# Optimization experiments

Hardware: AMD Instinct MI355X
Metric: run time of the kernel (lower is better)

The kernel has to match this reference:

```python
import jax, jax.numpy as jnp
import numpy as np

INPUT_SIZE = 416
NUM_CLASSES = 80
A = 3  # anchors per yolo layer
SS = [13, 26, 52]  # grid sizes (strides 32/16/8)
ANCHORS = [[(116, 90), (156, 198), (373, 326)],
           [(30, 61), (62, 45), (59, 119)],
           [(10, 13), (16, 30), (33, 23)]]
B, L = 16, 50


def _build_priors():
    boxes, cols, rows, pws, phs, szs = [], [], [], [], [], []
    for l, S in enumerate(SS):
        for i in range(S):
            for j in range(S):
                cx, cy = (j + 0.5) / S, (i + 0.5) / S
                for (aw, ah) in ANCHORS[l]:
                    w, h = aw / INPUT_SIZE, ah / INPUT_SIZE
                    boxes.append((cx - 0.5 * w, cy - 0.5 * h, w, h))
                    cols.append(j); rows.append(i)
                    pws.append(aw); phs.append(ah); szs.append(S)
    f = lambda a: np.asarray(a, np.float32)
    return f(boxes), f(cols), f(rows), f(pws), f(phs), f(szs)

PRIORS_NP, PCOL_NP, PROW_NP, PPW_NP, PPH_NP, PS_NP = _build_priors()
N = PRIORS_NP.shape[0]  # 10647
OFF = np.concatenate([[0], np.cumsum([S * S * A for S in SS])])


def setup_inputs() -> dict:
    key = jax.random.key(0)
    ks = jax.random.split(key, 8)
    inp = {}
    for l, S in enumerate(SS):
        inp[f"yolo_out{l}"] = jax.random.normal(ks[l], (B, A * (NUM_CLASSES + 5), S, S), jnp.float32)
    cls = jax.random.randint(ks[3], (B, L), 0, NUM_CLASSES).astype(jnp.float32)
    valid = jax.random.uniform(ks[4], (B, L)) < 0.4
    cls = jnp.where(valid, cls, -1.0)  # class < 0 means padding label
    xy = jax.random.uniform(ks[5], (B, L, 2), minval=0.0, maxval=0.7)
    wh = jax.random.uniform(ks[6], (B, L, 2), minval=0.05, maxval=0.3)
    inp["labels"] = jnp.concatenate([cls[..., None], xy, wh], axis=-1)[:, None]  # [B,1,L,5]
    return inp


def _bce(p, t):
    # torch BCELoss (mean) with the same log clamp at -100
    lg = lambda x: jnp.maximum(jnp.log(x), -100.0)
    return jnp.mean(-(t * lg(p) + (1.0 - t) * lg(1.0 - p)))


def _build_targets(labels):
    pri = jnp.asarray(PRIORS_NP)
    lab = labels[:, 0]  # [B,L,5]
    cls = lab[..., 0]
    valid = cls >= 0.0  # [B,L]
    bx, by, bw, bh = lab[..., 1], lab[..., 2], lab[..., 3], lab[..., 4]
    px, py, pw, ph = pri[:, 0], pri[:, 1], pri[:, 2], pri[:, 3]
    # IoU of every label against every prior: [B,L,N]
    ix = jnp.maximum(px, bx[..., None]); iy = jnp.maximum(py, by[..., None])
    ax = jnp.minimum(px + pw, (bx + bw)[..., None]); ay = jnp.minimum(py + ph, (by + bh)[..., None])
    inter = jnp.maximum(ax - ix, 0.0) * jnp.maximum(ay - iy, 0.0)
    ious = inter / (pw * ph + (bw * bh)[..., None] - inter)

    # priors with IoU>=0.5 to any gt are ignored for objectness (unless chosen as best)
    suppressed = jnp.any((ious >= 0.5) & valid[..., None], axis=1)  # [B,N]

    # best prior per label; on ties, pick the middle tied index (as the original)
    m = jnp.max(ious, axis=-1, keepdims=True)
    tie = ious == m
    k = tie.sum(-1)
    rank = (k - 1) // 2 + 1
    cs = jnp.cumsum(tie, -1)
    idx = jnp.argmax(tie & (cs == rank[..., None]), axis=-1)  # [B,L]

    colc = jnp.asarray(PCOL_NP)[idx]; rowc = jnp.asarray(PROW_NP)[idx]
    pwc = jnp.asarray(PPW_NP)[idx]; phc = jnp.asarray(PPH_NP)[idx]
    Sc = jnp.asarray(PS_NP)[idx]
    dx = jnp.clip((bx + 0.5 * bw) * Sc - colc, 1e-6, 0.999999)
    dy = jnp.clip((by + 0.5 * bh) * Sc - rowc, 1e-6, 0.999999)
    t_all = jnp.stack([jnp.log(dx / (1.0 - dx)), jnp.log(dy / (1.0 - dy)),
                       jnp.log(bw * INPUT_SIZE / pwc), jnp.log(bh * INPUT_SIZE / phc)], -1)  # [B,L,4]

    flat = (jnp.arange(B)[:, None] * N + idx).reshape(-1)  # [B*L]
    vflat = valid.reshape(-1)
    g = jnp.arange(B * L)
    winner = jax.ops.segment_max(jnp.where(vflat, g, -1), flat, num_segments=B * N)
    chosen = winner >= 0  # [B*N]
    coord_t = jnp.where(chosen[:, None], t_all.reshape(-1, 4)[jnp.clip(winner, 0)], 0.0)

    cls_i = jnp.where(vflat, cls.reshape(-1).astype(jnp.int32), 0)
    class_t = jnp.zeros((B * N, NUM_CLASSES), jnp.float32).at[flat, cls_i].max(vflat.astype(jnp.float32))

    obj_t = chosen.astype(jnp.float32).reshape(B, N)
    obj_m = (chosen.reshape(B, N) | ~suppressed).astype(jnp.float32)
    pos_m = chosen.astype(jnp.float32).reshape(B, N)
    return jax.lax.stop_gradient(
        (obj_t, obj_m, pos_m, coord_t.reshape(B, N, 4), class_t.reshape(B, N, NUM_CLASSES)))


def reference(yolo_out0, yolo_out1, yolo_out2, labels):
    obj_t, obj_m, pos_m, coord_t, class_t = _build_targets(labels)
    outs = [yolo_out0, yolo_out1, yolo_out2]
    Cp5 = NUM_CLASSES + 5
    obj_loss = coord_loss = class_loss = 0.0
    for l, S in enumerate(SS):
        n0, n1 = int(OFF[l]), int(OFF[l + 1])
        out = outs[l]
        # per-prior ordering within a layer is (row, col, anchor)
        om = obj_m[:, n0:n1].reshape(B, S, S, A).transpose(0, 3, 1, 2)
        ot = obj_t[:, n0:n1].reshape(B, S, S, A).transpose(0, 3, 1, 2)
        pm = pos_m[:, n0:n1].reshape(B, S, S, A)
        ct = coord_t[:, n0:n1].reshape(B, S, S, A, 4).transpose(0, 3, 4, 1, 2).reshape(B, A * 4, S, S)
        cm = jnp.broadcast_to(pm[..., None], (B, S, S, A, 4)).transpose(0, 3, 4, 1, 2).reshape(B, A * 4, S, S)
        kt = class_t[:, n0:n1].reshape(B, S, S, A, NUM_CLASSES).transpose(0, 3, 4, 1, 2).reshape(B, A * NUM_CLASSES, S, S)
        km = jnp.broadcast_to(pm[..., None], (B, S, S, A, NUM_CLASSES)).transpose(0, 3, 4, 1, 2).reshape(B, A * NUM_CLASSES, S, S)
        oi = np.arange(A) * Cp5 + 4
        ci = (np.arange(A)[:, None] * Cp5 + np.arange(4)).reshape(-1)
        ki = (np.arange(A)[:, None] * Cp5 + 5 + np.arange(NUM_CLASSES)).reshape(-1)
        obj_loss = obj_loss + _bce(jax.nn.sigmoid(out[:, oi]) * om, ot * om)
        coord_loss = coord_loss + jnp.mean((out[:, ci] * cm - ct * cm) ** 2)
        class_loss = class_loss + _bce(jax.nn.sigmoid(out[:, ki]) * km, kt * km)
    return jnp.stack([obj_loss, coord_loss, class_loss])
```

## Files before the change

### kernel.cpp

```cpp
#include <hip/hip_runtime.h>
#include <hip/hip_bf16.h>

#define NPRI 10647
#define BB 16
#define LL 50
#define OBJ_BLOCKS 666

__device__ __constant__ int c_AW[3][3] = {{116,156,373},{30,62,59},{10,16,33}};
__device__ __constant__ int c_AH[3][3] = {{90,198,326},{61,45,119},{23,30,23}};
__device__ __constant__ double c_wObj[3] = {1.0/8112.0, 1.0/32448.0, 1.0/129792.0};

__device__ inline void decode_prior(int n, int& level, int& S, int& ii, int& jj, int& aa) {
    int nn;
    if (n < 507)       { level = 0; S = 13; nn = n; }
    else if (n < 2535) { level = 1; S = 26; nn = n - 507; }
    else               { level = 2; S = 52; nn = n - 2535; }
    aa = nn % 3; int c = nn / 3; jj = c % S; ii = c / S;
}

__global__ __launch_bounds__(256) void init_kernel(
    float4* __restrict__ priorsA, float* __restrict__ priorsB,
    int* __restrict__ winner, unsigned char* __restrict__ supp,
    int* __restrict__ idxArr) {
    int i = blockIdx.x * 256 + threadIdx.x;
    if (i < BB * NPRI) { winner[i] = -1; supp[i] = 0; }
    if (i < BB * LL) idxArr[i] = -1;
    if (i < NPRI) {
        int level, S, ii, jj, aa;
        decode_prior(i, level, S, ii, jj, aa);
        double w  = (double)c_AW[level][aa] / 416.0;
        double h  = (double)c_AH[level][aa] / 416.0;
        double cx = ((double)jj + 0.5) / (double)S;
        double cy = ((double)ii + 0.5) / (double)S;
        float px = (float)(cx - 0.5 * w);
        float py = (float)(cy - 0.5 * h);
        float pw = (float)w, ph = (float)h;
        priorsA[i] = make_float4(px, py, __fadd_rn(px, pw), __fadd_rn(py, ph));
        priorsB[i] = __fmul_rn(pw, ph);
    }
}

__global__ __launch_bounds__(256) void assign_kernel(
    const float* __restrict__ labels, const float4* __restrict__ priorsA,
    const float* __restrict__ priorsB, int* __restrict__ winner,
    unsigned char* __restrict__ supp, int* __restrict__ idxArr,
    float4* __restrict__ tcoord) {
    __shared__ float s_iou[NPRI];
    __shared__ float s_red[256];
    __shared__ int   s_cnt[257];

    int b = blockIdx.x / LL, l = blockIdx.x % LL;
    const float* lab = labels + (b * LL + l) * 5;
    float cls = lab[0];
    if (cls < 0.0f) return;

    float bx = lab[1], by = lab[2], bw = lab[3], bh = lab[4];
    float bxe  = __fadd_rn(bx, bw), bye = __fadd_rn(by, bh);
    float bwbh = __fmul_rn(bw, bh);
    int tid = threadIdx.x;

    float lmax = -3.0e38f;
    for (int n = tid; n < NPRI; n += 256) {
        float4 p   = priorsA[n];
        float pwph = priorsB[n];
        float ix = fmaxf(p.x, bx), iy = fmaxf(p.y, by);
        float ax = fminf(p.z, bxe), ay = fminf(p.w, bye);
        float iw = fmaxf(__fsub_rn(ax, ix), 0.0f);
        float ih = fmaxf(__fsub_rn(ay, iy), 0.0f);
        float inter = __fmul_rn(iw, ih);
        float denom = __fsub_rn(__fadd_rn(pwph, bwbh), inter);
        float iou = __fdiv_rn(inter, denom);
        s_iou[n] = iou;
        lmax = fmaxf(lmax, iou);
        if (iou >= 0.5f) supp[b * NPRI + n] = 1;
    }
    s_red[tid] = lmax;
    __syncthreads();
    for (int s = 128; s > 0; s >>= 1) {
        if (tid < s) s_red[tid] = fmaxf(s_red[tid], s_red[tid + s]);
        __syncthreads();
    }
    float m = s_red[0];

    const int CH = 42;
    int start = tid * CH;
    int end   = min(start + CH, NPRI);
    int cnt = 0;
    for (int n = start; n < end; ++n) cnt += (s_iou[n] == m) ? 1 : 0;
    s_cnt[tid] = cnt;
    __syncthreads();
    if (tid == 0) {
        int acc = 0;
        for (int t = 0; t < 256; ++t) { int c = s_cnt[t]; s_cnt[t] = acc; acc += c; }
        s_cnt[256] = acc;
    }
    __syncthreads();
    int k    = s_cnt[256];
    int rank = (k - 1) / 2 + 1;
    int pre  = s_cnt[tid];
    if (pre < rank && rank <= pre + cnt) {
        int r = rank - pre;
        int sel = -1;
        for (int n = start; n < end; ++n) {
            if (s_iou[n] == m && --r == 0) { sel = n; break; }
        }
        int level, S, ii, jj, aa;
        decode_prior(sel, level, S, ii, jj, aa);
        float Sf = (float)S, colf = (float)jj, rowf = (float)ii;
        float awf = (float)c_AW[level][aa], ahf = (float)c_AH[level][aa];
        float dx = __fsub_rn(__fmul_rn(__fadd_rn(bx, __fmul_rn(0.5f, bw)), Sf), colf);
        float dy = __fsub_rn(__fmul_rn(__fadd_rn(by, __fmul_rn(0.5f, bh)), Sf), rowf);
        dx = fminf(fmaxf(dx, 1e-6f), 0.999999f);
        dy = fminf(fmaxf(dy, 1e-6f), 0.999999f);
        float t0 = logf(__fdiv_rn(dx, __fsub_rn(1.0f, dx)));
        float t1 = logf(__fdiv_rn(dy, __fsub_rn(1.0f, dy)));
        float t2 = logf(__fdiv_rn(__fmul_rn(bw, 416.0f), awf));
        float t3 = logf(__fdiv_rn(__fmul_rn(bh, 416.0f), ahf));
        int gi = b * LL + l;
        tcoord[gi] = make_float4(t0, t1, t2, t3);
        idxArr[gi] = sel;
        atomicMax(&winner[b * NPRI + sel], gi);
    }
}

__global__ __launch_bounds__(256) void obj_kernel(
    const float* __restrict__ o0, const float* __restrict__ o1, const float* __restrict__ o2,
    const int* __restrict__ winner, const unsigned char* __restrict__ supp,
    double* __restrict__ pObj) {
    int tid = threadIdx.x;
    int e = blockIdx.x * 256 + tid;
    double a = 0.0;
    if (e < BB * NPRI) {
        int b = e / NPRI, n = e % NPRI;
        int level, S, ii, jj, aa;
        decode_prior(n, level, S, ii, jj, aa);
        const float* out = (level == 0) ? o0 : ((level == 1) ? o1 : o2);
        int SS2 = S * S;
        float x = out[(size_t)b * 255 * SS2 + (aa * 85 + 4) * SS2 + ii * S + jj];
        bool chosen = (winner[e] >= 0);
        bool om = chosen || (supp[e] == 0);
        if (om) {
            float p = 1.0f / (1.0f + expf(-x));
            float t = chosen ? 1.0f : 0.0f;
            float lp = fmaxf(logf(p), -100.0f);
            float lq = fmaxf(logf(1.0f - p), -100.0f);
            a = -(double)(t * lp + (1.0f - t) * lq) * c_wObj[level];
        }
    }
    __shared__ double sred[256];
    sred[tid] = a; __syncthreads();
    for (int s = 128; s > 0; s >>= 1) { if (tid < s) sred[tid] += sred[tid + s]; __syncthreads(); }
    if (tid == 0) pObj[blockIdx.x] = sred[0];
}

__global__ __launch_bounds__(128) void chosen_kernel(
    const float* __restrict__ o0, const float* __restrict__ o1, const float* __restrict__ o2,
    const float* __restrict__ labels, const int* __restrict__ winner,
    const int* __restrict__ idxArr, const float4* __restrict__ tcoord,
    double* __restrict__ pCoord, double* __restrict__ pClass) {
    int gi = blockIdx.x;
    int tid = threadIdx.x;
    int b = gi / LL;
    int sel = idxArr[gi];
    bool active = (sel >= 0) && (winner[b * NPRI + sel] == gi);
    if (!active) {
        if (tid == 0) { pCoord[gi] = 0.0; pClass[gi] = 0.0; }
        return;
    }
    __shared__ int   s_idx[LL];
    __shared__ float s_cls[LL];
    __shared__ double s_red[128];
    if (tid < LL) {
        s_idx[tid] = idxArr[b * LL + tid];
        s_cls[tid] = labels[(b * LL + tid) * 5];
    }
    __syncthreads();

    int level, S, ii, jj, aa;
    decode_prior(sel, level, S, ii, jj, aa);
    int SS2 = S * S;
    const float* out = (level == 0) ? o0 : ((level == 1) ? o1 : o2);
    const float* base = out + (size_t)b * 255 * SS2 + aa * 85 * SS2 + ii * S + jj;
    double wObj = c_wObj[level];

    double val = 0.0;
    if (tid < 4) {
        float4 ct = tcoord[gi];
        float ctk = (tid == 0) ? ct.x : (tid == 1) ? ct.y : (tid == 2) ? ct.z : ct.w;
        float x = base[tid * SS2];
        float d = __fsub_rn(x, ctk);
        val = (double)__fmul_rn(d, d) * (wObj * 0.25);
    } else if (tid >= 5 && tid < 85) {
        int cc = tid - 5;
        float x = base[tid * SS2];
        float t = 0.0f;
        for (int l2 = 0; l2 < LL; ++l2)
            if (s_idx[l2] == sel && (int)s_cls[l2] == cc) t = 1.0f;
        float p = 1.0f / (1.0f + expf(-x));
        float lp = fmaxf(logf(p), -100.0f);
        float lq = fmaxf(logf(1.0f - p), -100.0f);
        val = -(double)(t * lp + (1.0f - t) * lq) * (wObj * 0.0125);
    }

    s_red[tid] = (tid < 4) ? val : 0.0;
    __syncthreads();
    for (int s = 64; s > 0; s >>= 1) { if (tid < s) s_red[tid] += s_red[tid + s]; __syncthreads(); }
    if (tid == 0) pCoord[gi] = s_red[0];
    __syncthreads();
    s_red[tid] = (tid >= 5 && tid < 85) ? val : 0.0;
    __syncthreads();
    for (int s = 64; s > 0; s >>= 1) { if (tid < s) s_red[tid] += s_red[tid + s]; __syncthreads(); }
    if (tid == 0) pClass[gi] = s_red[0];
}

__global__ __launch_bounds__(256) void finalize_kernel(
    const double* __restrict__ pObj, const double* __restrict__ pCoord,
    const double* __restrict__ pClass, float* __restrict__ out) {
    int tid = threadIdx.x;
    double sO = 0.0, sC = 0.0, sK = 0.0;
    for (int i = tid; i < OBJ_BLOCKS; i += 256) sO += pObj[i];
    for (int i = tid; i < BB * LL; i += 256) { sC += pCoord[i]; sK += pClass[i]; }
    __shared__ double r0[256], r1[256], r2[256];
    r0[tid] = sO; r1[tid] = sC; r2[tid] = sK;
    __syncthreads();
    for (int s = 128; s > 0; s >>= 1) {
        if (tid < s) { r0[tid] += r0[tid + s]; r1[tid] += r1[tid + s]; r2[tid] += r2[tid + s]; }
        __syncthreads();
    }
    if (tid == 0) { out[0] = (float)r0[0]; out[1] = (float)r1[0]; out[2] = (float)r2[0]; }
}

extern "C" void kernel_launch(void* const* d_in, const int* in_sizes, int n_in,
                              void* d_out, int out_size, void* d_ws, size_t ws_size,
                              hipStream_t stream) {
    const float* o0     = (const float*)d_in[0];
    const float* o1     = (const float*)d_in[1];
    const float* o2     = (const float*)d_in[2];
    const float* labels = (const float*)d_in[3];

    char* ws = (char*)d_ws;
    float4*        priorsA = (float4*)(ws);
    float*         priorsB = (float*) (ws + 170352);
    int*           winner  = (int*)   (ws + 212940);
    unsigned char* supp    = (unsigned char*)(ws + 894348);
    int*           idxArr  = (int*)   (ws + 1064700);
    float4*        tcoord  = (float4*)(ws + 1067904);
    double*        pObj    = (double*)(ws + 1080704);
    double*        pCoord  = (double*)(ws + 1086032);
    double*        pClass  = (double*)(ws + 1092432);

    int initBlocks = (BB * NPRI + 255) / 256;
    init_kernel<<<initBlocks, 256, 0, stream>>>(priorsA, priorsB, winner, supp, idxArr);
    assign_kernel<<<BB * LL, 256, 0, stream>>>(labels, priorsA, priorsB, winner, supp, idxArr, tcoord);
    obj_kernel<<<OBJ_BLOCKS, 256, 0, stream>>>(o0, o1, o2, winner, supp, pObj);
    chosen_kernel<<<BB * LL, 128, 0, stream>>>(o0, o1, o2, labels, winner, idxArr, tcoord, pCoord, pClass);
    finalize_kernel<<<1, 256, 0, stream>>>(pObj, pCoord, pClass, (float*)d_out);
}
```

Before: 128.8 us.

## Drop init kernel and winner/supp buffers; fuse obj and chosen loss kernels

Removes the init kernel and the global winner/suppression arrays. Priors are now computed on the fly from constants, suppression is recomputed in the objectness pass by looping over the batch's 50 labels, and the atomicMax winner is replaced by a last-index scan over idxArr. The objectness and chosen-prior loss kernels are merged into one launch with disjoint block ranges, and the serial prefix scan becomes a parallel Hillis-Steele scan. Kernel launches drop from five to three and global memory traffic shrinks, at the cost of recomputing 50 IoUs per prior-batch element in the loss kernel.

Result: no change. 127.0 us (-1.4%).

```diff
diff --git a/kernel.cpp b/kernel.cpp
--- a/kernel.cpp
+++ b/kernel.cpp
@@ -1,70 +1,78 @@
 #include <hip/hip_runtime.h>
-#include <hip/hip_bf16.h>
 
 #define NPRI 10647
 #define BB 16
 #define LL 50
 #define OBJ_BLOCKS 666
-
-__device__ __constant__ int c_AW[3][3] = {{116,156,373},{30,62,59},{10,16,33}};
-__device__ __constant__ int c_AH[3][3] = {{90,198,326},{61,45,119},{23,30,23}};
+#define CHO_BLOCKS (BB * LL)
+#define TOT_BLOCKS (OBJ_BLOCKS + CHO_BLOCKS)
+
+__device__ __constant__ double c_hw[3][3] = {
+    {0.5*(116.0/416.0), 0.5*(156.0/416.0), 0.5*(373.0/416.0)},
+    {0.5*( 30.0/416.0), 0.5*( 62.0/416.0), 0.5*( 59.0/416.0)},
+    {0.5*( 10.0/416.0), 0.5*( 16.0/416.0), 0.5*( 33.0/416.0)}};
+__device__ __constant__ double c_hh[3][3] = {
+    {0.5*( 90.0/416.0), 0.5*(198.0/416.0), 0.5*(326.0/416.0)},
+    {0.5*( 61.0/416.0), 0.5*( 45.0/416.0), 0.5*(119.0/416.0)},
+    {0.5*( 23.0/416.0), 0.5*( 30.0/416.0), 0.5*( 23.0/416.0)}};
+__device__ __constant__ float c_pwf[3][3] = {
+    {(float)(116.0/416.0), (float)(156.0/416.0), (float)(373.0/416.0)},
+    {(float)( 30.0/416.0), (float)( 62.0/416.0), (float)( 59.0/416.0)},
+    {(float)( 10.0/416.0), (float)( 16.0/416.0), (float)( 33.0/416.0)}};
+__device__ __constant__ float c_phf[3][3] = {
+    {(float)( 90.0/416.0), (float)(198.0/416.0), (float)(326.0/416.0)},
+    {(float)( 61.0/416.0), (float)( 45.0/416.0), (float)(119.0/416.0)},
+    {(float)( 23.0/416.0), (float)( 30.0/416.0), (float)( 23.0/416.0)}};
+__device__ __constant__ float c_awf[3][3] = {{116,156,373},{30,62,59},{10,16,33}};
+__device__ __constant__ float c_ahf[3][3] = {{90,198,326},{61,45,119},{23,30,23}};
 __device__ __constant__ double c_wObj[3] = {1.0/8112.0, 1.0/32448.0, 1.0/129792.0};
 
-__device__ inline void decode_prior(int n, int& level, int& S, int& ii, int& jj, int& aa) {
-    int nn;
-    if (n < 507)       { level = 0; S = 13; nn = n; }
-    else if (n < 2535) { level = 1; S = 26; nn = n - 507; }
-    else               { level = 2; S = 52; nn = n - 2535; }
-    aa = nn % 3; int c = nn / 3; jj = c % S; ii = c / S;
-}
-
-__global__ __launch_bounds__(256) void init_kernel(
-    float4* __restrict__ priorsA, float* __restrict__ priorsB,
-    int* __restrict__ winner, unsigned char* __restrict__ supp,
-    int* __restrict__ idxArr) {
-    int i = blockIdx.x * 256 + threadIdx.x;
-    if (i < BB * NPRI) { winner[i] = -1; supp[i] = 0; }
-    if (i < BB * LL) idxArr[i] = -1;
-    if (i < NPRI) {
-        int level, S, ii, jj, aa;
-        decode_prior(i, level, S, ii, jj, aa);
-        double w  = (double)c_AW[level][aa] / 416.0;
-        double h  = (double)c_AH[level][aa] / 416.0;
-        double cx = ((double)jj + 0.5) / (double)S;
-        double cy = ((double)ii + 0.5) / (double)S;
-        float px = (float)(cx - 0.5 * w);
-        float py = (float)(cy - 0.5 * h);
-        float pw = (float)w, ph = (float)h;
-        priorsA[i] = make_float4(px, py, __fadd_rn(px, pw), __fadd_rn(py, ph));
-        priorsB[i] = __fmul_rn(pw, ph);
-    }
+__device__ inline void decode_prior(int n, int& level, int& S, int& ii, int& jj,
+                                    int& aa, int& off) {
+    if (n < 507)        { level = 0; S = 13; int c = n / 3;            aa = n - 3*c;            jj = c % 13; ii = c / 13; off = 0;  }
+    else if (n < 2535)  { level = 1; S = 26; int nn = n - 507;  int c = nn / 3; aa = nn - 3*c; jj = c % 26; ii = c / 26; off = 13; }
+    else                { level = 2; S = 52; int nn = n - 2535; int c = nn / 3; aa = nn - 3*c; jj = c % 52; ii = c / 52; off = 39; }
 }
 
 __global__ __launch_bounds__(256) void assign_kernel(
-    const float* __restrict__ labels, const float4* __restrict__ priorsA,
-    const float* __restrict__ priorsB, int* __restrict__ winner,
-    unsigned char* __restrict__ supp, int* __restrict__ idxArr,
+    const float* __restrict__ labels, int* __restrict__ idxArr,
     float4* __restrict__ tcoord) {
-    __shared__ float s_iou[NPRI];
-    __shared__ float s_red[256];
-    __shared__ int   s_cnt[257];
-
-    int b = blockIdx.x / LL, l = blockIdx.x % LL;
-    const float* lab = labels + (b * LL + l) * 5;
+    __shared__ double s_cx[91];
+    __shared__ float  s_iou[NPRI];
+    __shared__ float  s_red[256];
+    __shared__ int    s_cnt[256];
+
+    int tid = threadIdx.x;
+    int gi  = blockIdx.x;
+    const float* lab = labels + gi * 5;
     float cls = lab[0];
+    if (tid == 0) idxArr[gi] = -1;
     if (cls < 0.0f) return;
+
+    if (tid < 91) {
+        int S, idx;
+        if (tid < 13)      { S = 13; idx = tid; }
+        else if (tid < 39) { S = 26; idx = tid - 13; }
+        else               { S = 52; idx = tid - 39; }
+        s_cx[tid] = ((double)idx + 0.5) / (double)S;
+    }
 
     float bx = lab[1], by = lab[2], bw = lab[3], bh = lab[4];
     float bxe  = __fadd_rn(bx, bw), bye = __fadd_rn(by, bh);
     float bwbh = __fmul_rn(bw, bh);
-    int tid = threadIdx.x;
+    __syncthreads();
 
     float lmax = -3.0e38f;
     for (int n = tid; n < NPRI; n += 256) {
-        float4 p   = priorsA[n];
-        float pwph = priorsB[n];
-        float ix = fmaxf(p.x, bx), iy = fmaxf(p.y, by);
-        float ax = fminf(p.z, bxe), ay = fminf(p.w, bye);
+        int level, S, ii, jj, aa, off;
+        decode_prior(n, level, S, ii, jj, aa, off);
+        float px  = (float)(s_cx[off + jj] - c_hw[level][aa]);
+        float py  = (float)(s_cx[off + ii] - c_hh[level][aa]);
+        float pwf = c_pwf[level][aa], phf = c_phf[level][aa];
+        float pxe = __fadd_rn(px, pwf), pye = __fadd_rn(py, phf);
+        float pwph = __fmul_rn(pwf, phf);
+        float ix = fmaxf(px, bx), iy = fmaxf(py, by);
+        float ax = fminf(pxe, bxe), ay = fminf(pye, bye);
         float iw = fmaxf(__fsub_rn(ax, ix), 0.0f);
         float ih = fmaxf(__fsub_rn(ay, iy), 0.0f);
         float inter = __fmul_rn(iw, ih);
@@ -72,7 +80,6 @@
         float iou = __fdiv_rn(inter, denom);
         s_iou[n] = iou;
         lmax = fmaxf(lmax, iou);
-        if (iou >= 0.5f) supp[b * NPRI + n] = 1;
     }
     s_red[tid] = lmax;
     __syncthreads();
@@ -87,130 +94,164 @@
     int end   = min(start + CH, NPRI);
     int cnt = 0;
     for (int n = start; n < end; ++n) cnt += (s_iou[n] == m) ? 1 : 0;
+
     s_cnt[tid] = cnt;
     __syncthreads();
-    if (tid == 0) {
-        int acc = 0;
-        for (int t = 0; t < 256; ++t) { int c = s_cnt[t]; s_cnt[t] = acc; acc += c; }
-        s_cnt[256] = acc;
-    }
-    __syncthreads();
-    int k    = s_cnt[256];
+    for (int d = 1; d < 256; d <<= 1) {
+        int add = (tid >= d) ? s_cnt[tid - d] : 0;
+        __syncthreads();
+        s_cnt[tid] += add;
+        __syncthreads();
+    }
+    int k    = s_cnt[255];
     int rank = (k - 1) / 2 + 1;
-    int pre  = s_cnt[tid];
+    int pre  = s_cnt[tid] - cnt;
+
     if (pre < rank && rank <= pre + cnt) {
         int r = rank - pre;
         int sel = -1;
-        for (int n = start; n < end; ++n) {
+        for (int n = start; n < end; ++n)
             if (s_iou[n] == m && --r == 0) { sel = n; break; }
-        }
-        int level, S, ii, jj, aa;
-        decode_prior(sel, level, S, ii, jj, aa);
+        int level, S, ii, jj, aa, off;
+        decode_prior(sel, level, S, ii, jj, aa, off);
         float Sf = (float)S, colf = (float)jj, rowf = (float)ii;
-        float awf = (float)c_AW[level][aa], ahf = (float)c_AH[level][aa];
         float dx = __fsub_rn(__fmul_rn(__fadd_rn(bx, __fmul_rn(0.5f, bw)), Sf), colf);
         float dy = __fsub_rn(__fmul_rn(__fadd_rn(by, __fmul_rn(0.5f, bh)), Sf), rowf);
         dx = fminf(fmaxf(dx, 1e-6f), 0.999999f);
         dy = fminf(fmaxf(dy, 1e-6f), 0.999999f);
         float t0 = logf(__fdiv_rn(dx, __fsub_rn(1.0f, dx)));
         float t1 = logf(__fdiv_rn(dy, __fsub_rn(1.0f, dy)));
-        float t2 = logf(__fdiv_rn(__fmul_rn(bw, 416.0f), awf));
-        float t3 = logf(__fdiv_rn(__fmul_rn(bh, 416.0f), ahf));
-        int gi = b * LL + l;
+        float t2 = logf(__fdiv_rn(__fmul_rn(bw, 416.0f), c_awf[level][aa]));
+        float t3 = logf(__fdiv_rn(__fmul_rn(bh, 416.0f), c_ahf[level][aa]));
         tcoord[gi] = make_float4(t0, t1, t2, t3);
         idxArr[gi] = sel;
-        atomicMax(&winner[b * NPRI + sel], gi);
-    }
-}
-
-__global__ __launch_bounds__(256) void obj_kernel(
+    }
+}
+
+__global__ __launch_bounds__(256) void loss_kernel(
     const float* __restrict__ o0, const float* __restrict__ o1, const float* __restrict__ o2,
-    const int* __restrict__ winner, const unsigned char* __restrict__ supp,
-    double* __restrict__ pObj) {
+    const float* __restrict__ labels, const int* __restrict__ idxArr,
+    const float4* __restrict__ tcoord,
+    double* __restrict__ pObj, double* __restrict__ pCoord, double* __restrict__ pClass) {
+    __shared__ float  s_box[2][LL][4];
+    __shared__ float  s_cls[2][LL];
+    __shared__ int    s_idx[2][LL];
+    __shared__ double s_red[256];
     int tid = threadIdx.x;
-    int e = blockIdx.x * 256 + tid;
-    double a = 0.0;
-    if (e < BB * NPRI) {
-        int b = e / NPRI, n = e % NPRI;
-        int level, S, ii, jj, aa;
-        decode_prior(n, level, S, ii, jj, aa);
+
+    if (blockIdx.x < OBJ_BLOCKS) {
+        int e0 = blockIdx.x * 256;
+        int b0 = e0 / NPRI;
+        int b1 = min((e0 + 255) / NPRI, BB - 1);
+        for (int t = tid; t < 2 * LL; t += 256) {
+            int which = t / LL, l = t - which * LL;
+            int b = which ? b1 : b0;
+            const float* lab = labels + (b * LL + l) * 5;
+            s_cls[which][l]    = lab[0];
+            s_box[which][l][0] = lab[1];
+            s_box[which][l][1] = lab[2];
+            s_box[which][l][2] = lab[3];
+            s_box[which][l][3] = lab[4];
+            s_idx[which][l]    = idxArr[b * LL + l];
+        }
+        __syncthreads();
+
+        int e = e0 + tid;
+        double a = 0.0;
+        if (e < BB * NPRI) {
+            int b = e / NPRI, n = e - b * NPRI;
+            int which = (b == b0) ? 0 : 1;
+            int level, S, ii, jj, aa, off;
+            decode_prior(n, level, S, ii, jj, aa, off);
+            double cxd = ((double)jj + 0.5) / (double)S;
+            double cyd = ((double)ii + 0.5) / (double)S;
+            float px  = (float)(cxd - c_hw[level][aa]);
+            float py  = (float)(cyd - c_hh[level][aa]);
+            float pwf = c_pwf[level][aa], phf = c_phf[level][aa];
+            float pxe = __fadd_rn(px, pwf), pye = __fadd_rn(py, phf);
+            float pwph = __fmul_rn(pwf, phf);
+            bool supp = false, chosen = false;
+            for (int l = 0; l < LL; ++l) {
+                if (s_cls[which][l] < 0.0f) continue;
+                if (s_idx[which][l] == n) chosen = true;
+                float bx = s_box[which][l][0], by = s_box[which][l][1];
+                float bw = s_box[which][l][2], bh = s_box[which][l][3];
+                float ix = fmaxf(px, bx), iy = fmaxf(py, by);
+                float ax = fminf(pxe, __fadd_rn(bx, bw));
+                float ay = fminf(pye, __fadd_rn(by, bh));
+                float iw = fmaxf(__fsub_rn(ax, ix), 0.0f);
+                float ih = fmaxf(__fsub_rn(ay, iy), 0.0f);
+                float inter = __fmul_rn(iw, ih);
+                float denom = __fsub_rn(__fadd_rn(pwph, __fmul_rn(bw, bh)), inter);
+                float iou = __fdiv_rn(inter, denom);
+                if (iou >= 0.5f) supp = true;
+            }
+            if (chosen || !supp) {
+                int SS2 = S * S;
+                const float* out = (level == 0) ? o0 : ((level == 1) ? o1 : o2);
+                float x = out[(size_t)b * 255 * SS2 + (aa * 85 + 4) * SS2 + ii * S + jj];
+                float p = 1.0f / (1.0f + expf(-x));
+                float t = chosen ? 1.0f : 0.0f;
+                float lp = fmaxf(logf(p), -100.0f);
+                float lq = fmaxf(logf(1.0f - p), -100.0f);
+                a = -(double)(t * lp + (1.0f - t) * lq) * c_wObj[level];
+            }
+        }
+        s_red[tid] = a; __syncthreads();
+        for (int s = 128; s > 0; s >>= 1) { if (tid < s) s_red[tid] += s_red[tid + s]; __syncthreads(); }
+        if (tid == 0) pObj[blockIdx.x] = s_red[0];
+    } else {
+        int gi = blockIdx.x - OBJ_BLOCKS;
+        int b  = gi / LL, lsel = gi - b * LL;
+        if (tid < LL) {
+            s_idx[0][tid] = idxArr[b * LL + tid];
+            s_cls[0][tid] = labels[(b * LL + tid) * 5];
+        }
+        __syncthreads();
+        int sel = s_idx[0][lsel];
+        int maxl = -1;
+        if (sel >= 0)
+            for (int l = 0; l < LL; ++l) if (s_idx[0][l] == sel) maxl = l;
+        bool active = (sel >= 0) && (maxl == lsel);
+        if (!active) {
+            if (tid == 0) { pCoord[gi] = 0.0; pClass[gi] = 0.0; }
+            return;
+        }
+        int level, S, ii, jj, aa, off;
+        decode_prior(sel, level, S, ii, jj, aa, off);
+        int SS2 = S * S;
         const float* out = (level == 0) ? o0 : ((level == 1) ? o1 : o2);
-        int SS2 = S * S;
-        float x = out[(size_t)b * 255 * SS2 + (aa * 85 + 4) * SS2 + ii * S + jj];
-        bool chosen = (winner[e] >= 0);
-        bool om = chosen || (supp[e] == 0);
-        if (om) {
+        const float* base = out + (size_t)b * 255 * SS2 + aa * 85 * SS2 + ii * S + jj;
+        double wObj = c_wObj[level];
+
+        double val = 0.0;
+        if (tid < 4) {
+            float4 ct = tcoord[gi];
+            float ctk = (tid == 0) ? ct.x : (tid == 1) ? ct.y : (tid == 2) ? ct.z : ct.w;
+            float x = base[tid * SS2];
+            float d = __fsub_rn(x, ctk);
+            val = (double)__fmul_rn(d, d) * (wObj * 0.25);
+        } else if (tid >= 5 && tid < 85) {
+            int cc = tid - 5;
+            float x = base[tid * SS2];
+            float t = 0.0f;
+            for (int l = 0; l < LL; ++l)
+                if (s_idx[0][l] == sel && (int)s_cls[0][l] == cc) t = 1.0f;
             float p = 1.0f / (1.0f + expf(-x));
-            float t = chosen ? 1.0f : 0.0f;
             float lp = fmaxf(logf(p), -100.0f);
             float lq = fmaxf(logf(1.0f - p), -100.0f);
-            a = -(double)(t * lp + (1.0f - t) * lq) * c_wObj[level];
-        }
-    }
-    __shared__ double sred[256];
-    sred[tid] = a; __syncthreads();
-    for (int s = 128; s > 0; s >>= 1) { if (tid < s) sred[tid] += sred[tid + s]; __syncthreads(); }
-    if (tid == 0) pObj[blockIdx.x] = sred[0];
-}
-
-__global__ __launch_bounds__(128) void chosen_kernel(
-    const float* __restrict__ o0, const float* __restrict__ o1, const float* __restrict__ o2,
-    const float* __restrict__ labels, const int* __restrict__ winner,
-    const int* __restrict__ idxArr, const float4* __restrict__ tcoord,
-    double* __restrict__ pCoord, double* __restrict__ pClass) {
-    int gi = blockIdx.x;
-    int tid = threadIdx.x;
-    int b = gi / LL;
-    int sel = idxArr[gi];
-    bool active = (sel >= 0) && (winner[b * NPRI + sel] == gi);
-    if (!active) {
-        if (tid == 0) { pCoord[gi] = 0.0; pClass[gi] = 0.0; }
-        return;
-    }
-    __shared__ int   s_idx[LL];
-    __shared__ float s_cls[LL];
-    __shared__ double s_red[128];
-    if (tid < LL) {
-        s_idx[tid] = idxArr[b * LL + tid];
-        s_cls[tid] = labels[(b * LL + tid) * 5];
-    }
-    __syncthreads();
-
-    int level, S, ii, jj, aa;
-    decode_prior(sel, level, S, ii, jj, aa);
-    int SS2 = S * S;
-    const float* out = (level == 0) ? o0 : ((level == 1) ? o1 : o2);
-    const float* base = out + (size_t)b * 255 * SS2 + aa * 85 * SS2 + ii * S + jj;
-    double wObj = c_wObj[level];
-
-    double val = 0.0;
-    if (tid < 4) {
-        float4 ct = tcoord[gi];
-        float ctk = (tid == 0) ? ct.x : (tid == 1) ? ct.y : (tid == 2) ? ct.z : ct.w;
-        float x = base[tid * SS2];
-        float d = __fsub_rn(x, ctk);
-        val = (double)__fmul_rn(d, d) * (wObj * 0.25);
-    } else if (tid >= 5 && tid < 85) {
-        int cc = tid - 5;
-        float x = base[tid * SS2];
-        float t = 0.0f;
-        for (int l2 = 0; l2 < LL; ++l2)
-            if (s_idx[l2] == sel && (int)s_cls[l2] == cc) t = 1.0f;
-        float p = 1.0f / (1.0f + expf(-x));
-        float lp = fmaxf(logf(p), -100.0f);
-        float lq = fmaxf(logf(1.0f - p), -100.0f);
-        val = -(double)(t * lp + (1.0f - t) * lq) * (wObj * 0.0125);
-    }
-
-    s_red[tid] = (tid < 4) ? val : 0.0;
-    __syncthreads();
-    for (int s = 64; s > 0; s >>= 1) { if (tid < s) s_red[tid] += s_red[tid + s]; __syncthreads(); }
-    if (tid == 0) pCoord[gi] = s_red[0];
-    __syncthreads();
-    s_red[tid] = (tid >= 5 && tid < 85) ? val : 0.0;
-    __syncthreads();
-    for (int s = 64; s > 0; s >>= 1) { if (tid < s) s_red[tid] += s_red[tid + s]; __syncthreads(); }
-    if (tid == 0) pClass[gi] = s_red[0];
+            val = -(double)(t * lp + (1.0f - t) * lq) * (wObj * 0.0125);
+        }
+        s_red[tid] = (tid < 4) ? val : 0.0;
+        __syncthreads();
+        for (int s = 128; s > 0; s >>= 1) { if (tid < s) s_red[tid] += s_red[tid + s]; __syncthreads(); }
+        if (tid == 0) pCoord[gi] = s_red[0];
+        __syncthreads();
+        s_red[tid] = (tid >= 5 && tid < 85) ? val : 0.0;
+        __syncthreads();
+        for (int s = 128; s > 0; s >>= 1) { if (tid < s) s_red[tid] += s_red[tid + s]; __syncthreads(); }
+        if (tid == 0) pClass[gi] = s_red[0];
+    }
 }
 
 __global__ __launch_bounds__(256) void finalize_kernel(
@@ -219,7 +260,7 @@
     int tid = threadIdx.x;
     double sO = 0.0, sC = 0.0, sK = 0.0;
     for (int i = tid; i < OBJ_BLOCKS; i += 256) sO += pObj[i];
-    for (int i = tid; i < BB * LL; i += 256) { sC += pCoord[i]; sK += pClass[i]; }
+    for (int i = tid; i < CHO_BLOCKS; i += 256) { sC += pCoord[i]; sK += pClass[i]; }
     __shared__ double r0[256], r1[256], r2[256];
     r0[tid] = sO; r1[tid] = sC; r2[tid] = sK;
     __syncthreads();
@@ -239,20 +280,14 @@
     const float* labels = (const float*)d_in[3];
 
     char* ws = (char*)d_ws;
-    float4*        priorsA = (float4*)(ws);
-    float*         priorsB = (float*) (ws + 170352);
-    int*           winner  = (int*)   (ws + 212940);
-    unsigned char* supp    = (unsigned char*)(ws + 894348);
-    int*           idxArr  = (int*)   (ws + 1064700);
-    float4*        tcoord  = (float4*)(ws + 1067904);
-    double*        pObj    = (double*)(ws + 1080704);
-    double*        pCoord  = (double*)(ws + 1086032);
-    double*        pClass  = (double*)(ws + 1092432);
-
-    int initBlocks = (BB * NPRI + 255) / 256;
-    init_kernel<<<initBlocks, 256, 0, stream>>>(priorsA, priorsB, winner, supp, idxArr);
-    assign_kernel<<<BB * LL, 256, 0, stream>>>(labels, priorsA, priorsB, winner, supp, idxArr, tcoord);
-    obj_kernel<<<OBJ_BLOCKS, 256, 0, stream>>>(o0, o1, o2, winner, supp, pObj);
-    chosen_kernel<<<BB * LL, 128, 0, stream>>>(o0, o1, o2, labels, winner, idxArr, tcoord, pCoord, pClass);
+    int*    idxArr = (int*)   (ws);
+    float4* tcoord = (float4*)(ws + 3200);
+    double* pObj   = (double*)(ws + 16000);
+    double* pCoord = (double*)(ws + 21328);
+    double* pClass = (double*)(ws + 27728);
+
+    assign_kernel<<<BB * LL, 256, 0, stream>>>(labels, idxArr, tcoord);
+    loss_kernel<<<TOT_BLOCKS, 256, 0, stream>>>(o0, o1, o2, labels, idxArr, tcoord,
+                                                pObj, pCoord, pClass);
     finalize_kernel<<<1, 256, 0, stream>>>(pObj, pCoord, pClass, (float*)d_out);
 }
```
